# Kernel tuning notes

Hardware: AMD Instinct MI355X
Metric: run time of the kernel (lower is better)

Reference implementation:

```python
import jax, jax.numpy as jnp
import numpy as np

STATE_SIZE, ACTION_SIZE, REWARD_SIZE = 128, 16, 4
IN = STATE_SIZE + REWARD_SIZE  # 132
B = 8192
W_NUM = 32


def _linear_params(key, fin, fout):
    k1, k2 = jax.random.split(key)
    s = 1.0 / np.sqrt(fin)
    w = jax.random.uniform(k1, (fout, fin), jnp.float32, -s, s)
    b = jax.random.uniform(k2, (fout,), jnp.float32, -s, s)
    return w, b


def setup_inputs() -> dict:
    key = jax.random.key(0)
    ks = jax.random.split(key, 7)
    w1, b1 = _linear_params(ks[0], IN, IN * 16)        # 132 -> 2112
    w2, b2 = _linear_params(ks[1], IN * 16, IN * 32)   # 2112 -> 4224
    w3, b3 = _linear_params(ks[2], IN * 32, IN * 64)   # 4224 -> 8448
    w4, b4 = _linear_params(ks[3], IN * 64, IN * 32)   # 8448 -> 4224
    wq, bq = _linear_params(ks[4], IN * 32, ACTION_SIZE * REWARD_SIZE)
    state = jax.random.normal(ks[5], (B, STATE_SIZE), jnp.float32)
    preference = jax.random.uniform(ks[6], (B, REWARD_SIZE), jnp.float32)
    return dict(state=state, preference=preference,
                w1=w1, b1=b1, w2=w2, b2=b2, w3=w3, b3=b3, w4=w4, b4=b4,
                wq=wq, bq=bq, w_num=W_NUM)


def _forward(state, preference, w1, b1, w2, b2, w3, b3, w4, b4, wq, bq, w_num):
    x = jnp.concatenate([state, preference], axis=1)              # [B, IN]
    h = jax.nn.relu(x @ w1.T + b1)
    h = jax.nn.relu(h @ w2.T + b2)
    h = jax.nn.relu(h @ w3.T + b3)
    h = jax.nn.relu(h @ w4.T + b4)
    q = (h @ wq.T + bq).reshape(-1, ACTION_SIZE, REWARD_SIZE)     # [B, A, R]

    s_num = preference.shape[0] // w_num
    # H(): envelope operator. The torch code repeat_interleaves flat_Q w_num
    # times per group; within each (w, s) group the preference vector is
    # constant, so inner products are constant across each run of w_num
    # repeated rows. argmax(dim=1)//w_num therefore equals argmax over the
    # action axis (first-tie semantics match). We compute that directly
    # without the O(w_num^2) blow-up -- identical math, identical output.
    qd = jax.lax.stop_gradient(q)                                 # Q.detach()
    rq = qd.reshape(s_num, w_num, ACTION_SIZE, REWARD_SIZE)
    rq = jnp.transpose(rq, (1, 0, 2, 3))                          # [w, s, A, R]
    rw = jnp.transpose(preference.reshape(s_num, w_num, REWARD_SIZE), (1, 0, 2))  # [w, s, R]
    ip = jnp.einsum('wsar,wsr->wsa', rq, rw)                      # [w, s, A]
    a_star = jnp.argmax(ip, axis=2)                               # [w, s]
    hq = jnp.take_along_axis(rq, a_star[..., None, None], axis=2)[:, :, 0, :]  # [w, s, R]
    hq = jnp.transpose(hq, (1, 0, 2)).reshape(-1, REWARD_SIZE)    # [s*w, R]
    return hq, q


def reference(state, preference, w1, b1, w2, b2, w3, b3, w4, b4, wq, bq, w_num):
    return _forward(state, preference, w1, b1, w2, b2, w3, b3, w4, b4, wq, bq, w_num)
```

## Files before the change

kernel.cpp:

```cpp
#include <hip/hip_runtime.h>


#define AS1 __attribute__((address_space(1)))
#define AS3 __attribute__((address_space(3)))

typedef _Float16 half8 __attribute__((ext_vector_type(8)));
typedef float floatx16 __attribute__((ext_vector_type(16)));

static constexpr float SCALE = 2048.0f;
static constexpr float INV_SCALE2 = 1.0f / (2048.0f * 2048.0f);

__global__ void split_w_kernel(const float* __restrict__ src, _Float16* __restrict__ hi,
                               _Float16* __restrict__ lo, int srcStride, int colOff,
                               int Kcopy, int Kpad) {
  int k = blockIdx.x * 256 + threadIdx.x;
  int n = blockIdx.y;
  if (k >= Kpad) return;
  float v = (k < Kcopy) ? src[(size_t)n * srcStride + colOff + k] * SCALE : 0.0f;
  _Float16 h = (_Float16)v;
  _Float16 l = (_Float16)(v - (float)h);
  size_t o = (size_t)n * Kpad + k;
  hi[o] = h;
  lo[o] = l;
}

__global__ void prep_x_kernel(const float* __restrict__ state, const float* __restrict__ pref,
                              _Float16* __restrict__ hi, _Float16* __restrict__ lo) {
  int k = threadIdx.x;
  int b = blockIdx.x;
  if (k >= 160) return;
  float v = 0.0f;
  if (k < 128) v = state[(size_t)b * 128 + k];
  else if (k < 132) v = pref[(size_t)b * 4 + (k - 128)];
  v *= SCALE;
  _Float16 h = (_Float16)v;
  _Float16 l = (_Float16)(v - (float)h);
  size_t o = (size_t)b * 160 + k;
  hi[o] = h;
  lo[o] = l;
}

__global__ __launch_bounds__(256) void gemm3_kernel(
    const _Float16* __restrict__ Ahi, const _Float16* __restrict__ Alo,
    const _Float16* __restrict__ Bhi, const _Float16* __restrict__ Blo,
    const float* __restrict__ bias,
    _Float16* __restrict__ Ohi, _Float16* __restrict__ Olo,
    float* __restrict__ Oacc,
    int K, int N, int kPerZ, int mode, int accAdd, int Mrows) {
  __shared__ _Float16 lds[4 * 4096];
  const int tid = threadIdx.x;
  const int wave = tid >> 6;
  const int lane = tid & 63;
  const int m0 = blockIdx.x * 128;
  const int n0 = blockIdx.y * 128;
  const int kBeg = blockIdx.z * kPerZ;

  const _Float16* gp[8];
  int loff[8];
#pragma unroll
  for (int j = 0; j < 8; ++j) {
    const int t = j >> 1;
    const int p = ((j & 1) << 8) + (wave << 6) + lane;
    const int r = p >> 2;
    const int g = (p & 3) ^ ((r >> 1) & 3);
    int row;
    const _Float16* plane;
    if (t < 2) {
      row = m0 + r;
      plane = t ? Alo : Ahi;
    } else {
      row = n0 + r;
      if (row > N - 1) row = N - 1;
      plane = (t == 3) ? Blo : Bhi;
    }
    gp[j] = plane + (size_t)row * K + kBeg + 8 * g;
    loff[j] = t * 4096 + (((j & 1) << 8) + (wave << 6)) * 8;
  }

  const int wm = wave >> 1, wn = wave & 1;
  floatx16 acc[2][2];
#pragma unroll
  for (int i = 0; i < 2; ++i)
#pragma unroll
    for (int j = 0; j < 2; ++j)
#pragma unroll
      for (int e = 0; e < 16; ++e) acc[i][j][e] = 0.0f;

  const int rA0 = (wm << 6) + (lane & 31);
  const int rB0 = (wn << 6) + (lane & 31);
  const int gHalf = lane >> 5;

  const int nSteps = kPerZ >> 5;
  for (int ks = 0; ks < nSteps; ++ks) {
    __syncthreads();
#pragma unroll
    for (int j = 0; j < 8; ++j) {
      __builtin_amdgcn_global_load_lds((const AS1 unsigned int*)gp[j],
                                       (AS3 unsigned int*)&lds[loff[j]], 16, 0, 0);
      gp[j] += 32;
    }
    __syncthreads();
#pragma unroll
    for (int kh = 0; kh < 2; ++kh) {
      half8 ah[2], al[2], bh[2], bl[2];
#pragma unroll
      for (int i = 0; i < 2; ++i) {
        int rA = rA0 + (i << 5);
        int sA = (rA << 2) + (((kh << 1) + gHalf) ^ ((rA >> 1) & 3));
        ah[i] = *(const half8*)&lds[sA << 3];
        al[i] = *(const half8*)&lds[4096 + (sA << 3)];
        int rB = rB0 + (i << 5);
        int sB = (rB << 2) + (((kh << 1) + gHalf) ^ ((rB >> 1) & 3));
        bh[i] = *(const half8*)&lds[8192 + (sB << 3)];
        bl[i] = *(const half8*)&lds[12288 + (sB << 3)];
      }
#pragma unroll
      for (int i = 0; i < 2; ++i)
#pragma unroll
        for (int j = 0; j < 2; ++j) {
          acc[i][j] = __builtin_amdgcn_mfma_f32_32x32x16_f16(ah[i], bh[j], acc[i][j], 0, 0, 0);
          acc[i][j] = __builtin_amdgcn_mfma_f32_32x32x16_f16(ah[i], bl[j], acc[i][j], 0, 0, 0);
          acc[i][j] = __builtin_amdgcn_mfma_f32_32x32x16_f16(al[i], bh[j], acc[i][j], 0, 0, 0);
        }
    }
  }

#pragma unroll
  for (int i = 0; i < 2; ++i)
#pragma unroll
    for (int j = 0; j < 2; ++j)
#pragma unroll
      for (int e = 0; e < 16; ++e) {
        int row = m0 + (wm << 6) + (i << 5) + ((e & 3) + ((e >> 2) << 3) + ((lane >> 5) << 2));
        int col = n0 + (wn << 6) + (j << 5) + (lane & 31);
        if (col < N) {
          float v = acc[i][j][e] * INV_SCALE2;
          if (mode == 0) {
            size_t o = (size_t)row * N + col;
            v = fmaxf(v + bias[col], 0.0f) * SCALE;
            _Float16 h = (_Float16)v;
            _Float16 l = (_Float16)(v - (float)h);
            Ohi[o] = h;
            Olo[o] = l;
          } else if (mode == 1) {
            size_t o = ((size_t)blockIdx.z * Mrows + row) * N + col;
            if (accAdd) v += Oacc[o];
            Oacc[o] = v;
          } else {
            size_t o = (size_t)row * N + col;
            v += Oacc[o];
            v = fmaxf(v + bias[col], 0.0f) * SCALE;
            _Float16 h = (_Float16)v;
            _Float16 l = (_Float16)(v - (float)h);
            Ohi[o] = h;
            Olo[o] = l;
          }
        }
      }
}

__global__ __launch_bounds__(128) void finish_kernel(
    const float* __restrict__ part, const float* __restrict__ bq,
    const float* __restrict__ pref, float* __restrict__ out, int rowBase, int Mc) {
  int b = blockIdx.x * 128 + threadIdx.x;
  if (b >= Mc) return;
  float q[64];
#pragma unroll
  for (int o4 = 0; o4 < 16; ++o4) {
    float4 s = *(const float4*)&part[(size_t)b * 64 + o4 * 4];
    float4 s1 = *(const float4*)&part[(size_t)(Mc + b) * 64 + o4 * 4];
    float4 s2 = *(const float4*)&part[(size_t)(2 * Mc + b) * 64 + o4 * 4];
    float4 s3 = *(const float4*)&part[(size_t)(3 * Mc + b) * 64 + o4 * 4];
    float4 bb = *(const float4*)&bq[o4 * 4];
    q[o4 * 4 + 0] = s.x + s1.x + s2.x + s3.x + bb.x;
    q[o4 * 4 + 1] = s.y + s1.y + s2.y + s3.y + bb.y;
    q[o4 * 4 + 2] = s.z + s1.z + s2.z + s3.z + bb.z;
    q[o4 * 4 + 3] = s.w + s1.w + s2.w + s3.w + bb.w;
  }
  int g = rowBase + b;
  float* qout = out + 32768 + (size_t)g * 64;
#pragma unroll
  for (int o4 = 0; o4 < 16; ++o4)
    *(float4*)&qout[o4 * 4] = make_float4(q[o4 * 4], q[o4 * 4 + 1], q[o4 * 4 + 2], q[o4 * 4 + 3]);
  float p0 = pref[(size_t)g * 4 + 0], p1 = pref[(size_t)g * 4 + 1];
  float p2 = pref[(size_t)g * 4 + 2], p3 = pref[(size_t)g * 4 + 3];
  float best = q[0] * p0 + q[1] * p1 + q[2] * p2 + q[3] * p3;
  int ba = 0;
#pragma unroll
  for (int a = 1; a < 16; ++a) {
    float ip = q[4 * a] * p0 + q[4 * a + 1] * p1 + q[4 * a + 2] * p2 + q[4 * a + 3] * p3;
    if (ip > best) { best = ip; ba = a; }
  }
  *(float4*)&out[(size_t)g * 4] =
      make_float4(q[4 * ba], q[4 * ba + 1], q[4 * ba + 2], q[4 * ba + 3]);
}

extern "C" void kernel_launch(void* const* d_in, const int* in_sizes, int n_in,
                              void* d_out, int out_size, void* d_ws, size_t ws_size,
                              hipStream_t stream) {
  const float* state = (const float*)d_in[0];
  const float* pref = (const float*)d_in[1];
  const float* w1 = (const float*)d_in[2];
  const float* b1 = (const float*)d_in[3];
  const float* w2 = (const float*)d_in[4];
  const float* b2 = (const float*)d_in[5];
  const float* w3 = (const float*)d_in[6];
  const float* b3 = (const float*)d_in[7];
  const float* w4 = (const float*)d_in[8];
  const float* b4 = (const float*)d_in[9];
  const float* wq = (const float*)d_in[10];
  const float* bq = (const float*)d_in[11];

  char* ws = (char*)d_ws;
  size_t off = 0;
  auto take = [&](size_t bytes) {
    size_t r = off;
    off += (bytes + 255) & ~(size_t)255;
    return r;
  };
  const size_t oW1h = take((size_t)2112 * 160 * 2);
  const size_t oW1l = take((size_t)2112 * 160 * 2);
  const size_t oW2h = take((size_t)4224 * 2112 * 2);
  const size_t oW2l = take((size_t)4224 * 2112 * 2);
  const size_t oW3h = take((size_t)2112 * 4224 * 2);
  const size_t oW3l = take((size_t)2112 * 4224 * 2);
  const size_t oW4h = take((size_t)4224 * 2112 * 2);
  const size_t oW4l = take((size_t)4224 * 2112 * 2);
  const size_t oW5h = take((size_t)64 * 4224 * 2);
  const size_t oW5l = take((size_t)64 * 4224 * 2);
  const size_t fixed = off;

  int Mc = 8192;
  while (Mc > 128 && fixed + (size_t)Mc * 51328 + 4096 > ws_size) Mc >>= 1;

  const size_t oXh = take((size_t)Mc * 160 * 2);
  const size_t oXl = take((size_t)Mc * 160 * 2);
  const size_t oH1h = take((size_t)Mc * 2112 * 2);
  const size_t oH1l = take((size_t)Mc * 2112 * 2);
  const size_t oH2h = take((size_t)Mc * 4224 * 2);
  const size_t oH2l = take((size_t)Mc * 4224 * 2);
  const size_t oH3h = take((size_t)Mc * 2112 * 2);
  const size_t oH3l = take((size_t)Mc * 2112 * 2);
  const size_t oACC = take((size_t)Mc * 4224 * 4);

  _Float16* W1h = (_Float16*)(ws + oW1h);
  _Float16* W1l = (_Float16*)(ws + oW1l);
  _Float16* W2h = (_Float16*)(ws + oW2h);
  _Float16* W2l = (_Float16*)(ws + oW2l);
  _Float16* W3h = (_Float16*)(ws + oW3h);
  _Float16* W3l = (_Float16*)(ws + oW3l);
  _Float16* W4h = (_Float16*)(ws + oW4h);
  _Float16* W4l = (_Float16*)(ws + oW4l);
  _Float16* W5h = (_Float16*)(ws + oW5h);
  _Float16* W5l = (_Float16*)(ws + oW5l);
  _Float16* Xh = (_Float16*)(ws + oXh);
  _Float16* Xl = (_Float16*)(ws + oXl);
  _Float16* H1h = (_Float16*)(ws + oH1h);
  _Float16* H1l = (_Float16*)(ws + oH1l);
  _Float16* H2h = (_Float16*)(ws + oH2h);
  _Float16* H2l = (_Float16*)(ws + oH2l);
  _Float16* H3h = (_Float16*)(ws + oH3h);
  _Float16* H3l = (_Float16*)(ws + oH3l);
  float* ACC = (float*)(ws + oACC);
  _Float16* H4h = H2h;
  _Float16* H4l = H2l;
  float* QP = (float*)(ws + oH1h);

  split_w_kernel<<<dim3(1, 2112), 256, 0, stream>>>(w1, W1h, W1l, 132, 0, 132, 160);
  split_w_kernel<<<dim3(9, 4224), 256, 0, stream>>>(w2, W2h, W2l, 2112, 0, 2112, 2112);
  split_w_kernel<<<dim3(17, 64), 256, 0, stream>>>(wq, W5h, W5l, 4224, 0, 4224, 4224);

  const int NC = 8192 / Mc;
  const int GX = Mc / 128;
  for (int mc = 0; mc < NC; ++mc) {
    const float* st = state + (size_t)mc * Mc * 128;
    const float* pf = pref + (size_t)mc * Mc * 4;
    prep_x_kernel<<<dim3(Mc), 192, 0, stream>>>(st, pf, Xh, Xl);
    gemm3_kernel<<<dim3(GX, 17), 256, 0, stream>>>(Xh, Xl, W1h, W1l, b1, H1h, H1l,
                                                   nullptr, 160, 2112, 160, 0, 0, Mc);
    gemm3_kernel<<<dim3(GX, 33), 256, 0, stream>>>(H1h, H1l, W2h, W2l, b2, H2h, H2l,
                                                   nullptr, 2112, 4224, 2112, 0, 0, Mc);
    for (int c = 0; c < 4; ++c) {
      split_w_kernel<<<dim3(17, 2112), 256, 0, stream>>>(w3 + (size_t)c * 2112 * 4224, W3h,
                                                         W3l, 4224, 0, 4224, 4224);
      split_w_kernel<<<dim3(9, 4224), 256, 0, stream>>>(w4, W4h, W4l, 8448, c * 2112, 2112,
                                                        2112);
      gemm3_kernel<<<dim3(GX, 17), 256, 0, stream>>>(H2h, H2l, W3h, W3l, b3 + c * 2112,
                                                     H3h, H3l, nullptr, 4224, 2112, 4224,
                                                     0, 0, Mc);
      if (c < 3) {
        gemm3_kernel<<<dim3(GX, 33), 256, 0, stream>>>(H3h, H3l, W4h, W4l, nullptr, nullptr,
                                                       nullptr, ACC, 2112, 4224, 2112, 1,
                                                       c > 0 ? 1 : 0, Mc);
      } else {
        gemm3_kernel<<<dim3(GX, 33), 256, 0, stream>>>(H3h, H3l, W4h, W4l, b4, H4h, H4l,
                                                       ACC, 2112, 4224, 2112, 2, 0, Mc);
      }
    }
    gemm3_kernel<<<dim3(GX, 1, 4), 256, 0, stream>>>(H4h, H4l, W5h, W5l, nullptr, nullptr,
                                                     nullptr, QP, 4224, 64, 1056, 1, 0, Mc);
    finish_kernel<<<dim3(Mc / 128), 128, 0, stream>>>(QP, bq, pref, (float*)d_out,
                                                      mc * Mc, Mc);
  }
}
```

Measured before the change: 5.334 ms.

## Enlarge GEMM tile to 256x128 with 512 threads and triple-buffered async LDS loads

The split-fp16 GEMM kernel moves from a 128x128 tile with 256 threads to a 256x128 tile with 512 threads (8 waves). The single-buffered load/sync/compute loop becomes a three-stage ring of LDS buffers fed by global_load_lds, with vmcnt waits, split half-step prefetches and s_setprio around the MFMA blocks. The goal is to overlap global-to-LDS transfers with MFMA work and to reuse each B tile across more rows. In exchange the kernel uses much more LDS, which may limit occupancy, and the minimum chunk size rises to 256 rows.

```diff
diff --git a/kernel.cpp b/kernel.cpp
--- a/kernel.cpp
+++ b/kernel.cpp
@@ -40,41 +40,46 @@
   lo[o] = l;
 }
 
-__global__ __launch_bounds__(256) void gemm3_kernel(
+__global__ __launch_bounds__(512) void gemm3_kernel(
     const _Float16* __restrict__ Ahi, const _Float16* __restrict__ Alo,
     const _Float16* __restrict__ Bhi, const _Float16* __restrict__ Blo,
     const float* __restrict__ bias,
     _Float16* __restrict__ Ohi, _Float16* __restrict__ Olo,
     float* __restrict__ Oacc,
     int K, int N, int kPerZ, int mode, int accAdd, int Mrows) {
-  __shared__ _Float16 lds[4 * 4096];
+  __shared__ __attribute__((aligned(16))) _Float16 lds[3 * 24576];
   const int tid = threadIdx.x;
   const int wave = tid >> 6;
   const int lane = tid & 63;
-  const int m0 = blockIdx.x * 128;
+  const int m0 = blockIdx.x * 256;
   const int n0 = blockIdx.y * 128;
   const int kBeg = blockIdx.z * kPerZ;
 
-  const _Float16* gp[8];
-  int loff[8];
-#pragma unroll
-  for (int j = 0; j < 8; ++j) {
-    const int t = j >> 1;
-    const int p = ((j & 1) << 8) + (wave << 6) + lane;
+  const _Float16* gp[6];
+  int ldsoff[6];
+#pragma unroll
+  for (int j = 0; j < 6; ++j) {
+    int q = j * 512 + tid;
+    int plane, p;
+    if (q < 1024)      { plane = 0; p = q; }
+    else if (q < 2048) { plane = 1; p = q - 1024; }
+    else if (q < 2560) { plane = 2; p = q - 2048; }
+    else               { plane = 3; p = q - 2560; }
     const int r = p >> 2;
     const int g = (p & 3) ^ ((r >> 1) & 3);
     int row;
-    const _Float16* plane;
-    if (t < 2) {
+    const _Float16* ptr;
+    if (plane < 2) {
       row = m0 + r;
-      plane = t ? Alo : Ahi;
+      ptr = plane ? Alo : Ahi;
     } else {
       row = n0 + r;
       if (row > N - 1) row = N - 1;
-      plane = (t == 3) ? Blo : Bhi;
-    }
-    gp[j] = plane + (size_t)row * K + kBeg + 8 * g;
-    loff[j] = t * 4096 + (((j & 1) << 8) + (wave << 6)) * 8;
+      ptr = (plane == 3) ? Blo : Bhi;
+    }
+    gp[j] = ptr + (size_t)row * K + kBeg + 8 * g;
+    int pbase = (plane == 0) ? 0 : (plane == 1) ? 8192 : (plane == 2) ? 16384 : 20480;
+    ldsoff[j] = pbase + (p & ~63) * 8;
   }
 
   const int wm = wave >> 1, wn = wave & 1;
@@ -89,41 +94,84 @@
   const int rA0 = (wm << 6) + (lane & 31);
   const int rB0 = (wn << 6) + (lane & 31);
   const int gHalf = lane >> 5;
-
-  const int nSteps = kPerZ >> 5;
-  for (int ks = 0; ks < nSteps; ++ks) {
-    __syncthreads();
-#pragma unroll
-    for (int j = 0; j < 8; ++j) {
-      __builtin_amdgcn_global_load_lds((const AS1 unsigned int*)gp[j],
-                                       (AS3 unsigned int*)&lds[loff[j]], 16, 0, 0);
-      gp[j] += 32;
-    }
-    __syncthreads();
-#pragma unroll
-    for (int kh = 0; kh < 2; ++kh) {
-      half8 ah[2], al[2], bh[2], bl[2];
-#pragma unroll
-      for (int i = 0; i < 2; ++i) {
-        int rA = rA0 + (i << 5);
-        int sA = (rA << 2) + (((kh << 1) + gHalf) ^ ((rA >> 1) & 3));
-        ah[i] = *(const half8*)&lds[sA << 3];
-        al[i] = *(const half8*)&lds[4096 + (sA << 3)];
-        int rB = rB0 + (i << 5);
-        int sB = (rB << 2) + (((kh << 1) + gHalf) ^ ((rB >> 1) & 3));
-        bh[i] = *(const half8*)&lds[8192 + (sB << 3)];
-        bl[i] = *(const half8*)&lds[12288 + (sB << 3)];
+  const int nT = kPerZ >> 5;
+
+#define STAGEJ(J0, J1, BUF)                                                        \
+  {                                                                                \
+    const int bo_ = (BUF) * 24576;                                                 \
+    _Pragma("unroll") for (int j = (J0); j <= (J1); ++j) {                         \
+      __builtin_amdgcn_global_load_lds((const AS1 unsigned int*)gp[j],             \
+                                       (AS3 unsigned int*)&lds[bo_ + ldsoff[j]],   \
+                                       16, 0, 0);                                  \
+      gp[j] += 32;                                                                 \
+    }                                                                              \
+  }
+
+  STAGEJ(0, 5, 0)
+  if (nT > 1) STAGEJ(0, 5, 1)
+
+  int cb = 0, pb = 2;
+  for (int t = 0; t < nT; ++t) {
+    if (t + 1 < nT) {
+      asm volatile("s_waitcnt vmcnt(6)" ::: "memory");
+    } else {
+      asm volatile("s_waitcnt vmcnt(0)" ::: "memory");
+    }
+    __builtin_amdgcn_s_barrier();
+    const int bo = cb * 24576;
+
+    half8 ah[2], al[2], bh[2], bl[2];
+    if (t + 2 < nT) STAGEJ(0, 2, pb)
+#pragma unroll
+    for (int i = 0; i < 2; ++i) {
+      int rA = rA0 + (i << 5);
+      int sA = (rA << 2) + (gHalf ^ ((rA >> 1) & 3));
+      ah[i] = *(const half8*)&lds[bo + sA * 8];
+      al[i] = *(const half8*)&lds[bo + 8192 + sA * 8];
+      int rB = rB0 + (i << 5);
+      int sB = (rB << 2) + (gHalf ^ ((rB >> 1) & 3));
+      bh[i] = *(const half8*)&lds[bo + 16384 + sB * 8];
+      bl[i] = *(const half8*)&lds[bo + 20480 + sB * 8];
+    }
+    __builtin_amdgcn_s_setprio(1);
+#pragma unroll
+    for (int i = 0; i < 2; ++i)
+#pragma unroll
+      for (int j = 0; j < 2; ++j) {
+        acc[i][j] = __builtin_amdgcn_mfma_f32_32x32x16_f16(ah[i], bh[j], acc[i][j], 0, 0, 0);
+        acc[i][j] = __builtin_amdgcn_mfma_f32_32x32x16_f16(ah[i], bl[j], acc[i][j], 0, 0, 0);
+        acc[i][j] = __builtin_amdgcn_mfma_f32_32x32x16_f16(al[i], bh[j], acc[i][j], 0, 0, 0);
       }
-#pragma unroll
-      for (int i = 0; i < 2; ++i)
-#pragma unroll
-        for (int j = 0; j < 2; ++j) {
-          acc[i][j] = __builtin_amdgcn_mfma_f32_32x32x16_f16(ah[i], bh[j], acc[i][j], 0, 0, 0);
-          acc[i][j] = __builtin_amdgcn_mfma_f32_32x32x16_f16(ah[i], bl[j], acc[i][j], 0, 0, 0);
-          acc[i][j] = __builtin_amdgcn_mfma_f32_32x32x16_f16(al[i], bh[j], acc[i][j], 0, 0, 0);
-        }
-    }
-  }
+    __builtin_amdgcn_s_setprio(0);
+    __builtin_amdgcn_s_barrier();
+
+    if (t + 2 < nT) STAGEJ(3, 5, pb)
+#pragma unroll
+    for (int i = 0; i < 2; ++i) {
+      int rA = rA0 + (i << 5);
+      int sA = (rA << 2) + ((2 + gHalf) ^ ((rA >> 1) & 3));
+      ah[i] = *(const half8*)&lds[bo + sA * 8];
+      al[i] = *(const half8*)&lds[bo + 8192 + sA * 8];
+      int rB = rB0 + (i << 5);
+      int sB = (rB << 2) + ((2 + gHalf) ^ ((rB >> 1) & 3));
+      bh[i] = *(const half8*)&lds[bo + 16384 + sB * 8];
+      bl[i] = *(const half8*)&lds[bo + 20480 + sB * 8];
+    }
+    __builtin_amdgcn_s_setprio(1);
+#pragma unroll
+    for (int i = 0; i < 2; ++i)
+#pragma unroll
+      for (int j = 0; j < 2; ++j) {
+        acc[i][j] = __builtin_amdgcn_mfma_f32_32x32x16_f16(ah[i], bh[j], acc[i][j], 0, 0, 0);
+        acc[i][j] = __builtin_amdgcn_mfma_f32_32x32x16_f16(ah[i], bl[j], acc[i][j], 0, 0, 0);
+        acc[i][j] = __builtin_amdgcn_mfma_f32_32x32x16_f16(al[i], bh[j], acc[i][j], 0, 0, 0);
+      }
+    __builtin_amdgcn_s_setprio(0);
+
+    cb = (cb == 2) ? 0 : cb + 1;
+    pb = (pb == 2) ? 0 : pb + 1;
+  }
+#undef STAGEJ
 
 #pragma unroll
   for (int i = 0; i < 2; ++i)
@@ -231,7 +279,7 @@
   const size_t fixed = off;
 
   int Mc = 8192;
-  while (Mc > 128 && fixed + (size_t)Mc * 51328 + 4096 > ws_size) Mc >>= 1;
+  while (Mc > 256 && fixed + (size_t)Mc * 51328 + 4096 > ws_size) Mc >>= 1;
 
   const size_t oXh = take((size_t)Mc * 160 * 2);
   const size_t oXl = take((size_t)Mc * 160 * 2);
@@ -271,33 +319,33 @@
   split_w_kernel<<<dim3(17, 64), 256, 0, stream>>>(wq, W5h, W5l, 4224, 0, 4224, 4224);
 
   const int NC = 8192 / Mc;
-  const int GX = Mc / 128;
+  const int GX = Mc / 256;
   for (int mc = 0; mc < NC; ++mc) {
     const float* st = state + (size_t)mc * Mc * 128;
     const float* pf = pref + (size_t)mc * Mc * 4;
     prep_x_kernel<<<dim3(Mc), 192, 0, stream>>>(st, pf, Xh, Xl);
-    gemm3_kernel<<<dim3(GX, 17), 256, 0, stream>>>(Xh, Xl, W1h, W1l, b1, H1h, H1l,
+    gemm3_kernel<<<dim3(GX, 17), 512, 0, stream>>>(Xh, Xl, W1h, W1l, b1, H1h, H1l,
                                                    nullptr, 160, 2112, 160, 0, 0, Mc);
-    gemm3_kernel<<<dim3(GX, 33), 256, 0, stream>>>(H1h, H1l, W2h, W2l, b2, H2h, H2l,
+    gemm3_kernel<<<dim3(GX, 33), 512, 0, stream>>>(H1h, H1l, W2h, W2l, b2, H2h, H2l,
                                                    nullptr, 2112, 4224, 2112, 0, 0, Mc);
     for (int c = 0; c < 4; ++c) {
       split_w_kernel<<<dim3(17, 2112), 256, 0, stream>>>(w3 + (size_t)c * 2112 * 4224, W3h,
                                                          W3l, 4224, 0, 4224, 4224);
       split_w_kernel<<<dim3(9, 4224), 256, 0, stream>>>(w4, W4h, W4l, 8448, c * 2112, 2112,
                                                         2112);
-      gemm3_kernel<<<dim3(GX, 17), 256, 0, stream>>>(H2h, H2l, W3h, W3l, b3 + c * 2112,
+      gemm3_kernel<<<dim3(GX, 17), 512, 0, stream>>>(H2h, H2l, W3h, W3l, b3 + c * 2112,
                                                      H3h, H3l, nullptr, 4224, 2112, 4224,
                                                      0, 0, Mc);
       if (c < 3) {
-        gemm3_kernel<<<dim3(GX, 33), 256, 0, stream>>>(H3h, H3l, W4h, W4l, nullptr, nullptr,
+        gemm3_kernel<<<dim3(GX, 33), 512, 0, stream>>>(H3h, H3l, W4h, W4l, nullptr, nullptr,
                                                        nullptr, ACC, 2112, 4224, 2112, 1,
                                                        c > 0 ? 1 : 0, Mc);
       } else {
-        gemm3_kernel<<<dim3(GX, 33), 256, 0, stream>>>(H3h, H3l, W4h, W4l, b4, H4h, H4l,
+        gemm3_kernel<<<dim3(GX, 33), 512, 0, stream>>>(H3h, H3l, W4h, W4l, b4, H4h, H4l,
                                                        ACC, 2112, 4224, 2112, 2, 0, Mc);
       }
     }
-    gemm3_kernel<<<dim3(GX, 1, 4), 256, 0, stream>>>(H4h, H4l, W5h, W5l, nullptr, nullptr,
+    gemm3_kernel<<<dim3(GX, 1, 4), 512, 0, stream>>>(H4h, H4l, W5h, W5l, nullptr, nullptr,
                                                      nullptr, QP, 4224, 64, 1056, 1, 0, Mc);
     finish_kernel<<<dim3(Mc / 128), 128, 0, stream>>>(QP, bq, pref, (float*)d_out,
                                                       mc * Mc, Mc);
```

Result: slower. 5.810 ms (+8.9%).

## Double-buffer LDS tiles with async global-to-LDS prefetch in split-fp16 GEMM

Applied to the files above, without the earlier changes.

Replaces the load-sync-compute GEMM main loop with a two-buffer LDS pipeline. The next K-tile is fetched by global_load_lds while the current one feeds MFMA, using fine-grained vmcnt waits and raised wave priority around the MFMA blocks. The LDS layout is reorganised so each k-half forms a contiguous sub-tile with a new XOR swizzle. The goal is to hide global memory latency and remove the exposed barrier stalls, at the cost of twice the LDS per block, which may lower occupancy.

```diff
diff --git a/kernel.cpp b/kernel.cpp
--- a/kernel.cpp
+++ b/kernel.cpp
@@ -47,7 +47,7 @@
     _Float16* __restrict__ Ohi, _Float16* __restrict__ Olo,
     float* __restrict__ Oacc,
     int K, int N, int kPerZ, int mode, int accAdd, int Mrows) {
-  __shared__ _Float16 lds[4 * 4096];
+  __shared__ __attribute__((aligned(16))) _Float16 lds[2 * 16384];
   const int tid = threadIdx.x;
   const int wave = tid >> 6;
   const int lane = tid & 63;
@@ -61,20 +61,22 @@
   for (int j = 0; j < 8; ++j) {
     const int t = j >> 1;
     const int p = ((j & 1) << 8) + (wave << 6) + lane;
-    const int r = p >> 2;
-    const int g = (p & 3) ^ ((r >> 1) & 3);
+    const int kh = p >> 8;
+    const int rr = (p & 255) >> 1;
+    const int q = p & 1;
+    const int G = (kh << 1) | (q ^ ((rr >> 2) & 1));
     int row;
     const _Float16* plane;
     if (t < 2) {
-      row = m0 + r;
+      row = m0 + rr;
       plane = t ? Alo : Ahi;
     } else {
-      row = n0 + r;
+      row = n0 + rr;
       if (row > N - 1) row = N - 1;
       plane = (t == 3) ? Blo : Bhi;
     }
-    gp[j] = plane + (size_t)row * K + kBeg + 8 * g;
-    loff[j] = t * 4096 + (((j & 1) << 8) + (wave << 6)) * 8;
+    gp[j] = plane + (size_t)row * K + kBeg + 8 * G;
+    loff[j] = t * 4096 + (p & ~63) * 8;
   }
 
   const int wm = wave >> 1, wn = wave & 1;
@@ -89,41 +91,82 @@
   const int rA0 = (wm << 6) + (lane & 31);
   const int rB0 = (wn << 6) + (lane & 31);
   const int gHalf = lane >> 5;
-
-  const int nSteps = kPerZ >> 5;
-  for (int ks = 0; ks < nSteps; ++ks) {
-    __syncthreads();
-#pragma unroll
-    for (int j = 0; j < 8; ++j) {
-      __builtin_amdgcn_global_load_lds((const AS1 unsigned int*)gp[j],
-                                       (AS3 unsigned int*)&lds[loff[j]], 16, 0, 0);
-      gp[j] += 32;
-    }
-    __syncthreads();
-#pragma unroll
-    for (int kh = 0; kh < 2; ++kh) {
-      half8 ah[2], al[2], bh[2], bl[2];
-#pragma unroll
-      for (int i = 0; i < 2; ++i) {
-        int rA = rA0 + (i << 5);
-        int sA = (rA << 2) + (((kh << 1) + gHalf) ^ ((rA >> 1) & 3));
-        ah[i] = *(const half8*)&lds[sA << 3];
-        al[i] = *(const half8*)&lds[4096 + (sA << 3)];
-        int rB = rB0 + (i << 5);
-        int sB = (rB << 2) + (((kh << 1) + gHalf) ^ ((rB >> 1) & 3));
-        bh[i] = *(const half8*)&lds[8192 + (sB << 3)];
-        bl[i] = *(const half8*)&lds[12288 + (sB << 3)];
+  const int nT = kPerZ >> 5;
+
+#define STAGE_G(PAR, BUF)                                                          \
+  {                                                                                \
+    const int bo_ = (BUF);                                                         \
+    _Pragma("unroll") for (int j = (PAR); j < 8; j += 2) {                         \
+      __builtin_amdgcn_global_load_lds((const AS1 unsigned int*)gp[j],             \
+                                       (AS3 unsigned int*)&lds[bo_ + loff[j]],     \
+                                       16, 0, 0);                                  \
+      gp[j] += 32;                                                                 \
+    }                                                                              \
+  }
+
+  STAGE_G(0, 0)
+  STAGE_G(1, 0)
+
+  for (int t = 0; t < nT; ++t) {
+    const int bo = (t & 1) << 14;
+    const int po = 16384 - bo;
+
+    asm volatile("s_waitcnt vmcnt(4)" ::: "memory");
+    __builtin_amdgcn_s_barrier();
+    half8 ah[2], al[2], bh[2], bl[2];
+#pragma unroll
+    for (int i = 0; i < 2; ++i) {
+      int rA = rA0 + (i << 5);
+      int sA = (rA << 1) + (gHalf ^ ((rA >> 2) & 1));
+      ah[i] = *(const half8*)&lds[bo + (sA << 3)];
+      al[i] = *(const half8*)&lds[bo + 4096 + (sA << 3)];
+      int rB = rB0 + (i << 5);
+      int sB = (rB << 1) + (gHalf ^ ((rB >> 2) & 1));
+      bh[i] = *(const half8*)&lds[bo + 8192 + (sB << 3)];
+      bl[i] = *(const half8*)&lds[bo + 12288 + (sB << 3)];
+    }
+    if (t + 1 < nT) STAGE_G(0, po)
+    __builtin_amdgcn_s_setprio(1);
+#pragma unroll
+    for (int i = 0; i < 2; ++i)
+#pragma unroll
+      for (int j = 0; j < 2; ++j) {
+        acc[i][j] = __builtin_amdgcn_mfma_f32_32x32x16_f16(ah[i], bh[j], acc[i][j], 0, 0, 0);
+        acc[i][j] = __builtin_amdgcn_mfma_f32_32x32x16_f16(ah[i], bl[j], acc[i][j], 0, 0, 0);
+        acc[i][j] = __builtin_amdgcn_mfma_f32_32x32x16_f16(al[i], bh[j], acc[i][j], 0, 0, 0);
       }
-#pragma unroll
-      for (int i = 0; i < 2; ++i)
-#pragma unroll
-        for (int j = 0; j < 2; ++j) {
-          acc[i][j] = __builtin_amdgcn_mfma_f32_32x32x16_f16(ah[i], bh[j], acc[i][j], 0, 0, 0);
-          acc[i][j] = __builtin_amdgcn_mfma_f32_32x32x16_f16(ah[i], bl[j], acc[i][j], 0, 0, 0);
-          acc[i][j] = __builtin_amdgcn_mfma_f32_32x32x16_f16(al[i], bh[j], acc[i][j], 0, 0, 0);
-        }
-    }
-  }
+    __builtin_amdgcn_s_setprio(0);
+
+    if (t + 1 < nT) {
+      asm volatile("s_waitcnt vmcnt(4)" ::: "memory");
+    } else {
+      asm volatile("s_waitcnt vmcnt(0)" ::: "memory");
+    }
+    __builtin_amdgcn_s_barrier();
+#pragma unroll
+    for (int i = 0; i < 2; ++i) {
+      int rA = rA0 + (i << 5);
+      int sA = 256 + (rA << 1) + (gHalf ^ ((rA >> 2) & 1));
+      ah[i] = *(const half8*)&lds[bo + (sA << 3)];
+      al[i] = *(const half8*)&lds[bo + 4096 + (sA << 3)];
+      int rB = rB0 + (i << 5);
+      int sB = 256 + (rB << 1) + (gHalf ^ ((rB >> 2) & 1));
+      bh[i] = *(const half8*)&lds[bo + 8192 + (sB << 3)];
+      bl[i] = *(const half8*)&lds[bo + 12288 + (sB << 3)];
+    }
+    if (t + 1 < nT) STAGE_G(1, po)
+    __builtin_amdgcn_s_setprio(1);
+#pragma unroll
+    for (int i = 0; i < 2; ++i)
+#pragma unroll
+      for (int j = 0; j < 2; ++j) {
+        acc[i][j] = __builtin_amdgcn_mfma_f32_32x32x16_f16(ah[i], bh[j], acc[i][j], 0, 0, 0);
+        acc[i][j] = __builtin_amdgcn_mfma_f32_32x32x16_f16(ah[i], bl[j], acc[i][j], 0, 0, 0);
+        acc[i][j] = __builtin_amdgcn_mfma_f32_32x32x16_f16(al[i], bh[j], acc[i][j], 0, 0, 0);
+      }
+    __builtin_amdgcn_s_setprio(0);
+  }
+#undef STAGE_G
 
 #pragma unroll
   for (int i = 0; i < 2; ++i)
```

Result: slower. 6.658 ms (+24.8%).
